# Kernel tuning notes

Hardware: AMD Instinct MI355X
Metric: run time of the kernel (lower is better)

## Reference

```python
import jax, jax.numpy as jnp
import numpy as np

D = 128
EPS = 1e-6


def setup_inputs() -> dict:
    key = jax.random.key(0)
    k1, k2, k3, k4 = jax.random.split(key, 4)
    N, NQ, NK = 32, 2048, 2048
    queries = jax.random.normal(k1, (N, NQ, D), dtype=jnp.float32)
    keys = jax.random.normal(k2, (N, NK, D), dtype=jnp.float32)
    values = jax.random.normal(k3, (N, NK, D), dtype=jnp.float32)
    # multiplicative (soft) mask in [0,1)
    mask = jax.random.uniform(k4, (N, NQ, NK), dtype=jnp.float32)
    return {"queries": queries, "keys": keys, "values": values, "mask": mask}


def reference(queries, keys, values, mask):
    # scaled dot-product scores: N x n_q x n_k
    scaled = jnp.einsum("bqd,bkd->bqk", queries, keys) / jnp.sqrt(jnp.float32(D))
    attn = jax.nn.softmax(scaled, axis=2)
    # post-softmax multiplicative masking + renormalization
    attn = attn * mask
    attn = attn / (jnp.sum(attn, axis=2, keepdims=True) + EPS)
    return jnp.einsum("bqk,bkd->bqd", attn, values)
```

## Files before the change

kernel.cpp:

```cpp
#include <hip/hip_runtime.h>

#define NB   32
#define NQL  2048
#define NKL  2048
#define DH   128
#define QBLK 128
#define KBLK 64
#define NT   (NKL / KBLK)
#define EPS  1e-6f

typedef __bf16 bf16x8 __attribute__((ext_vector_type(8)));
typedef __bf16 bf16x4 __attribute__((ext_vector_type(4)));
typedef float  f32x4  __attribute__((ext_vector_type(4)));

__global__ __launch_bounds__(256) void
prep_kv(const float* __restrict__ Kg, const float* __restrict__ Vg,
        unsigned short* __restrict__ Kimg, unsigned short* __restrict__ Vimg)
{
    __shared__ float T[64 * 132];
    const int t = threadIdx.x;
    if (blockIdx.x < NB * NT) {
        const int blk = blockIdx.x;
        const int rK  = t >> 2;
        const int x0  = (t & 3) * 32;
        const int swz = (rK & 7) << 3;
        const float* src = Kg + ((size_t)blk * 64 + rK) * DH;
        unsigned short* dst = Kimg + ((size_t)blk << 13) + rK * 128;
        #pragma unroll
        for (int i = 0; i < 4; ++i) {
            const int c0 = (x0 + i * 8) ^ swz;
            float4 a = *(const float4*)(src + c0);
            float4 c = *(const float4*)(src + c0 + 4);
            *(bf16x8*)(dst + x0 + i * 8) =
                (bf16x8){ (__bf16)a.x, (__bf16)a.y, (__bf16)a.z, (__bf16)a.w,
                          (__bf16)c.x, (__bf16)c.y, (__bf16)c.z, (__bf16)c.w };
        }
    } else {
        const int blk = blockIdx.x - NB * NT;
        {
            const int r  = t >> 2;
            const int c0 = (t & 3) * 32;
            const float* src = Vg + ((size_t)blk * 64 + r) * DH + c0;
            #pragma unroll
            for (int j = 0; j < 8; ++j)
                *(float4*)&T[r * 132 + c0 + j * 4] = *(const float4*)(src + j * 4);
        }
        __syncthreads();
        {
            const int dV  = t >> 1;
            const int yh  = (t & 1) * 32;
            const int swz = (dV & 7) << 3;
            unsigned short* dst = Vimg + ((size_t)blk << 13) + dV * 64 + yh;
            #pragma unroll
            for (int i = 0; i < 4; ++i) {
                const int ks = (yh + i * 8) ^ swz;
                bf16x8 o;
                #pragma unroll
                for (int j = 0; j < 8; ++j) o[j] = (__bf16)T[(ks + j) * 132 + dV];
                *(bf16x8*)(dst + i * 8) = o;
            }
        }
    }
}


#define GLL16(GSRC, LDST) \
    __builtin_amdgcn_global_load_lds( \
        (const __attribute__((address_space(1))) void*)(GSRC), \
        (__attribute__((address_space(3))) void*)(LDST), 16, 0, 0)

#define ISSUE_KV(KT, KB_, VB_) do { \
    const size_t tb_ = ((size_t)(b * 32 + (KT))) << 14; \
    const char* ksrc_ = KimgB + tb_ + woff + lby; \
    const char* vsrc_ = VimgB + tb_ + woff + lby; \
    char* kd_ = (char*)(KB_) + woff; \
    char* vd_ = (char*)(VB_) + woff; \
    GLL16(ksrc_ +    0, kd_ +    0);  GLL16(ksrc_ + 1024, kd_ + 1024); \
    GLL16(vsrc_ +    0, vd_ +    0);  GLL16(vsrc_ + 1024, vd_ + 1024); \
} while (0)

#define LOAD_M(K0, R0, R1, R2, R3) do { \
    const float* mb_ = mbase + (K0); \
    R0 = *(const float4*)(mb_ +  0);  R1 = *(const float4*)(mb_ + 16); \
    R2 = *(const float4*)(mb_ + 32);  R3 = *(const float4*)(mb_ + 48); \
} while (0)

#define COMPUTE(KB, VB, M0, M1, M2, M3) do { \
    f32x4 sacc[4]; \
    _Pragma("unroll") for (int m = 0; m < 4; ++m) sacc[m] = (f32x4){0.f,0.f,0.f,0.f}; \
    __builtin_amdgcn_s_setprio(1); \
    _Pragma("unroll") for (int m = 0; m < 4; ++m) { \
        _Pragma("unroll") for (int c = 0; c < 4; ++c) { \
            bf16x8 af = *(bf16x8*)&KB[(m * 16 + lq) * 128 + ((c * 32 + lg * 8) ^ swzL)]; \
            sacc[m] = __builtin_amdgcn_mfma_f32_16x16x32_bf16(af, qf[c], sacc[m], 0, 0, 0); \
        } \
    } \
    __builtin_amdgcn_s_setprio(0); \
    float mk_[16] = { M0.x, M0.y, M0.z, M0.w,  M1.x, M1.y, M1.z, M1.w, \
                      M2.x, M2.y, M2.z, M2.w,  M3.x, M3.y, M3.z, M3.w }; \
    float sv[4][4], tmax = -1e30f; \
    _Pragma("unroll") for (int m = 0; m < 4; ++m) \
        _Pragma("unroll") for (int r = 0; r < 4; ++r) { \
            sv[m][r] = sacc[m][r] * scale; \
            tmax = fmaxf(tmax, sv[m][r]); \
        } \
    tmax = fmaxf(tmax, __shfl_xor(tmax, 16)); \
    tmax = fmaxf(tmax, __shfl_xor(tmax, 32)); \
    if (!__all(tmax - m_run <= 8.f)) { \
        const float mnew_  = fmaxf(m_run, tmax); \
        const float alpha_ = __expf(m_run - mnew_); \
        m_run = mnew_;  z_part *= alpha_;  s_part *= alpha_; \
        float alr[4]; \
        _Pragma("unroll") for (int r = 0; r < 4; ++r) alr[r] = __shfl(alpha_, lg * 4 + r); \
        _Pragma("unroll") for (int n = 0; n < 8; ++n) \
            _Pragma("unroll") for (int r = 0; r < 4; ++r) oacc[n][r] *= alr[r]; \
    } \
    float zl = 0.f, sl = 0.f, pm[4][4]; \
    _Pragma("unroll") for (int m = 0; m < 4; ++m) \
        _Pragma("unroll") for (int r = 0; r < 4; ++r) { \
            float p = __expf(sv[m][r] - m_run); \
            zl += p; \
            float pq = p * mk_[m * 4 + r]; \
            sl += pq;  pm[m][r] = pq; \
        } \
    z_part += zl;  s_part += sl; \
    _Pragma("unroll") for (int kc = 0; kc < 2; ++kc) { \
        *(bf16x4*)&Ps[w][lq][lg * 4] = \
            (bf16x4){ (__bf16)pm[2*kc][0], (__bf16)pm[2*kc][1], \
                      (__bf16)pm[2*kc][2], (__bf16)pm[2*kc][3] }; \
        *(bf16x4*)&Ps[w][lq][16 + lg * 4] = \
            (bf16x4){ (__bf16)pm[2*kc+1][0], (__bf16)pm[2*kc+1][1], \
                      (__bf16)pm[2*kc+1][2], (__bf16)pm[2*kc+1][3] }; \
        bf16x8 pa = *(bf16x8*)&Ps[w][lq][lg * 8]; \
        __builtin_amdgcn_s_setprio(1); \
        _Pragma("unroll") for (int n = 0; n < 8; ++n) { \
            bf16x8 vv = *(bf16x8*)&VB[(n * 16 + lq) * 64 + ((kc * 32 + lg * 8) ^ swzL)]; \
            oacc[n] = __builtin_amdgcn_mfma_f32_16x16x32_bf16(pa, vv, oacc[n], 0, 0, 0); \
        } \
        __builtin_amdgcn_s_setprio(0); \
    } \
} while (0)

#define ITER(KT, KBc, VBc, KBn, VBn, MU0,MU1,MU2,MU3, ML0,ML1,ML2,ML3, LAST) do { \
    if (!(LAST)) { \
        ISSUE_KV((KT) + 1, KBn, VBn); \
        LOAD_M(((KT) + 1) * KBLK, ML0, ML1, ML2, ML3); \
    } \
    __builtin_amdgcn_sched_barrier(0); \
    COMPUTE(KBc, VBc, MU0, MU1, MU2, MU3); \
    if (!(LAST)) __syncthreads(); \
} while (0)

__global__ __launch_bounds__(512, 4) void
attn_main(const float* __restrict__ Qg, const unsigned short* __restrict__ Kimg,
          const unsigned short* __restrict__ Vimg, const float* __restrict__ Mg,
          float* __restrict__ Og)
{
    const int wg = ((blockIdx.x & 7) << 6) | (blockIdx.x >> 3);
    const int b  = wg >> 4;
    const int qt = wg & 15;

    const int t  = threadIdx.x;
    const int w  = t >> 6;
    const int l  = t & 63;
    const int lq = l & 15;
    const int lg = l >> 4;
    const int swzL = (lq & 7) << 3;
    const int woff = w * 2048;
    const int lby  = l * 16;

    __shared__ __align__(16) unsigned short Kb0[64 * 128];
    __shared__ __align__(16) unsigned short Kb1[64 * 128];
    __shared__ __align__(16) unsigned short Vb0[128 * 64];
    __shared__ __align__(16) unsigned short Vb1[128 * 64];
    __shared__ __align__(16) unsigned short Ps[8][16][40];

    const char* KimgB = (const char*)Kimg;
    const char* VimgB = (const char*)Vimg;

    const int qrow = qt * QBLK + w * 16 + lq;

    bf16x8 qf[4];
    {
        const float* qb = Qg + ((size_t)b * NQL + qrow) * DH;
        #pragma unroll
        for (int c = 0; c < 4; ++c) {
            const float* p = qb + c * 32 + lg * 8;
            float4 x = *(const float4*)(p);
            float4 y = *(const float4*)(p + 4);
            qf[c] = (bf16x8){ (__bf16)x.x, (__bf16)x.y, (__bf16)x.z, (__bf16)x.w,
                              (__bf16)y.x, (__bf16)y.y, (__bf16)y.z, (__bf16)y.w };
        }
    }

    float m_run = -1e30f, z_part = 0.f, s_part = 0.f;
    f32x4 oacc[8];
    #pragma unroll
    for (int n = 0; n < 8; ++n) oacc[n] = (f32x4){0.f, 0.f, 0.f, 0.f};

    const float* mbase = Mg + ((size_t)b * NQL + qrow) * NKL + lg * 4;
    const float scale = 0.08838834764831845f;

    float4 mA0, mA1, mA2, mA3, mB0, mB1, mB2, mB3;

    ISSUE_KV(0, Kb0, Vb0);
    LOAD_M(0, mA0, mA1, mA2, mA3);
    __syncthreads();

    for (int kt = 0; kt < NT - 2; kt += 2) {
        ITER(kt,     Kb0, Vb0, Kb1, Vb1, mA0,mA1,mA2,mA3, mB0,mB1,mB2,mB3, 0);
        ITER(kt + 1, Kb1, Vb1, Kb0, Vb0, mB0,mB1,mB2,mB3, mA0,mA1,mA2,mA3, 0);
    }
    ITER(NT - 2, Kb0, Vb0, Kb1, Vb1, mA0,mA1,mA2,mA3, mB0,mB1,mB2,mB3, 0);
    ITER(NT - 1, Kb1, Vb1, Kb0, Vb0, mB0,mB1,mB2,mB3, mA0,mA1,mA2,mA3, 1);

    float z = z_part + __shfl_xor(z_part, 16);
    z += __shfl_xor(z, 32);
    float s = s_part + __shfl_xor(s_part, 16);
    s += __shfl_xor(s, 32);
    const float inv = 1.f / (s + EPS * z);
    float ivr[4];
    #pragma unroll
    for (int r = 0; r < 4; ++r) ivr[r] = __shfl(inv, lg * 4 + r);

    float* ob = Og + ((size_t)b * NQL + qt * QBLK + w * 16) * DH;
    #pragma unroll
    for (int n = 0; n < 8; ++n)
        #pragma unroll
        for (int r = 0; r < 4; ++r)
            ob[(size_t)(lg * 4 + r) * DH + n * 16 + lq] = oacc[n][r] * ivr[r];
}

__global__ __launch_bounds__(256, 3) void
attn_fb(const float* __restrict__ Qg, const float* __restrict__ Kg,
        const float* __restrict__ Vg, const float* __restrict__ Mg,
        float* __restrict__ Og)
{
    const int wg = ((blockIdx.x & 7) << 7) | (blockIdx.x >> 3);
    const int b  = wg >> 5;
    const int q0 = (wg & 31) * 64;
    const int t  = threadIdx.x;
    const int w  = t >> 6;
    const int l  = t & 63;
    const int lq = l & 15;
    const int lg = l >> 4;
    __shared__ __align__(16) unsigned short Ks[64 * 128];
    __shared__ __align__(16) unsigned short Vs[128 * 64];
    __shared__ __align__(16) unsigned short Ps[4][16][72];
    const int rK   = t >> 2;
    const int cK   = (t & 3) * 32;
    const int dV   = t >> 1;
    const int khV  = t & 1;
    const int swzK = (rK & 7) << 3;
    const int swzV = (dV & 7) << 3;
    const int swzL = (lq & 7) << 3;
    const int qrow = q0 + w * 16 + lq;
    bf16x8 qf[4];
    {
        const float* qb = Qg + ((size_t)b * NQL + qrow) * DH;
        #pragma unroll
        for (int c = 0; c < 4; ++c) {
            const float* p = qb + c * 32 + lg * 8;
            float4 x = *(const float4*)(p);
            float4 y = *(const float4*)(p + 4);
            qf[c] = (bf16x8){ (__bf16)x.x, (__bf16)x.y, (__bf16)x.z, (__bf16)x.w,
                              (__bf16)y.x, (__bf16)y.y, (__bf16)y.z, (__bf16)y.w };
        }
    }
    float m_run = -1e30f, z_part = 0.f, s_part = 0.f;
    f32x4 oacc[8];
    #pragma unroll
    for (int n = 0; n < 8; ++n) oacc[n] = (f32x4){0.f, 0.f, 0.f, 0.f};
    const float* kbase = Kg + (size_t)b * NKL * DH;
    const float* vbase = Vg + (size_t)b * NKL * DH;
    const float* mbase = Mg + ((size_t)b * NQL + qrow) * NKL;
    const float scale = 0.08838834764831845f;
    for (int kt = 0; kt < NT; ++kt) {
        const int k0 = kt * KBLK;
        float mkf[16];
        {
            const float* mb = mbase + k0 + lg * 4;
            #pragma unroll
            for (int m = 0; m < 4; ++m) {
                float4 x = *(const float4*)(mb + m * 16);
                mkf[m*4+0]=x.x; mkf[m*4+1]=x.y; mkf[m*4+2]=x.z; mkf[m*4+3]=x.w;
            }
        }
        __syncthreads();
        {
            const float* kb = kbase + (size_t)(k0 + rK) * DH + cK;
            #pragma unroll
            for (int i = 0; i < 4; ++i) {
                float4 a = *(const float4*)(kb + i * 8);
                float4 c = *(const float4*)(kb + i * 8 + 4);
                *(bf16x8*)&Ks[rK * 128 + ((cK + i * 8) ^ swzK)] =
                    (bf16x8){ (__bf16)a.x, (__bf16)a.y, (__bf16)a.z, (__bf16)a.w,
                              (__bf16)c.x, (__bf16)c.y, (__bf16)c.z, (__bf16)c.w };
            }
            const float* vb = vbase + (size_t)(k0 + khV * 32) * DH + dV;
            #pragma unroll
            for (int i = 0; i < 4; ++i) {
                bf16x8 o;
                #pragma unroll
                for (int j = 0; j < 8; ++j) o[j] = (__bf16)vb[(i * 8 + j) * DH];
                *(bf16x8*)&Vs[dV * 64 + (((khV << 5) + i * 8) ^ swzV)] = o;
            }
        }
        __syncthreads();
        f32x4 sacc[4];
        #pragma unroll
        for (int m = 0; m < 4; ++m) sacc[m] = (f32x4){0.f,0.f,0.f,0.f};
        #pragma unroll
        for (int m = 0; m < 4; ++m)
            #pragma unroll
            for (int c = 0; c < 4; ++c) {
                bf16x8 af = *(bf16x8*)&Ks[(m * 16 + lq) * 128 + ((c * 32 + lg * 8) ^ swzL)];
                sacc[m] = __builtin_amdgcn_mfma_f32_16x16x32_bf16(af, qf[c], sacc[m], 0, 0, 0);
            }
        float sv[4][4], tmax = -1e30f;
        #pragma unroll
        for (int m = 0; m < 4; ++m)
            #pragma unroll
            for (int r = 0; r < 4; ++r) {
                sv[m][r] = sacc[m][r] * scale;
                tmax = fmaxf(tmax, sv[m][r]);
            }
        tmax = fmaxf(tmax, __shfl_xor(tmax, 16));
        tmax = fmaxf(tmax, __shfl_xor(tmax, 32));
        if (!__all(tmax - m_run <= 8.f)) {
            const float mnew  = fmaxf(m_run, tmax);
            const float alpha = __expf(m_run - mnew);
            m_run = mnew; z_part *= alpha; s_part *= alpha;
            float alr[4];
            #pragma unroll
            for (int r = 0; r < 4; ++r) alr[r] = __shfl(alpha, lg * 4 + r);
            #pragma unroll
            for (int n = 0; n < 8; ++n)
                #pragma unroll
                for (int r = 0; r < 4; ++r) oacc[n][r] *= alr[r];
        }
        float zl = 0.f, sl = 0.f, pm[4][4];
        #pragma unroll
        for (int m = 0; m < 4; ++m)
            #pragma unroll
            for (int r = 0; r < 4; ++r) {
                float p = __expf(sv[m][r] - m_run);
                zl += p;
                float pq = p * mkf[m * 4 + r];
                sl += pq; pm[m][r] = pq;
            }
        z_part += zl; s_part += sl;
        #pragma unroll
        for (int m = 0; m < 4; ++m)
            *(bf16x4*)&Ps[w][lq][m * 16 + lg * 4] =
                (bf16x4){ (__bf16)pm[m][0], (__bf16)pm[m][1], (__bf16)pm[m][2], (__bf16)pm[m][3] };
        #pragma unroll
        for (int kc = 0; kc < 2; ++kc) {
            bf16x8 pa = *(bf16x8*)&Ps[w][lq][kc * 32 + lg * 8];
            #pragma unroll
            for (int n = 0; n < 8; ++n) {
                bf16x8 vv = *(bf16x8*)&Vs[(n * 16 + lq) * 64 + ((kc * 32 + lg * 8) ^ swzL)];
                oacc[n] = __builtin_amdgcn_mfma_f32_16x16x32_bf16(pa, vv, oacc[n], 0, 0, 0);
            }
        }
    }
    float z = z_part + __shfl_xor(z_part, 16);
    z += __shfl_xor(z, 32);
    float s = s_part + __shfl_xor(s_part, 16);
    s += __shfl_xor(s, 32);
    const float inv = 1.f / (s + EPS * z);
    float ivr[4];
    #pragma unroll
    for (int r = 0; r < 4; ++r) ivr[r] = __shfl(inv, lg * 4 + r);
    float* ob = Og + ((size_t)b * NQL + q0 + w * 16) * DH;
    #pragma unroll
    for (int n = 0; n < 8; ++n)
        #pragma unroll
        for (int r = 0; r < 4; ++r)
            ob[(size_t)(lg * 4 + r) * DH + n * 16 + lq] = oacc[n][r] * ivr[r];
}

extern "C" void kernel_launch(void* const* d_in, const int* in_sizes, int n_in,
                              void* d_out, int out_size, void* d_ws, size_t ws_size,
                              hipStream_t stream)
{
    (void)in_sizes; (void)n_in; (void)out_size;
    const float* Q = (const float*)d_in[0];
    const float* K = (const float*)d_in[1];
    const float* V = (const float*)d_in[2];
    const float* M = (const float*)d_in[3];
    float* O = (float*)d_out;

    const size_t imgElems = (size_t)NB * NKL * DH;
    const size_t need     = 2 * imgElems * sizeof(unsigned short);

    if (ws_size >= need) {
        unsigned short* Kimg = (unsigned short*)d_ws;
        unsigned short* Vimg = Kimg + imgElems;
        prep_kv<<<dim3(2 * NB * NT), 256, 0, stream>>>(K, V, Kimg, Vimg);
        attn_main<<<dim3(NB * (NQL / QBLK)), 512, 0, stream>>>(Q, Kimg, Vimg, M, O);
    } else {
        attn_fb<<<dim3(NB * (NQL / 64)), 256, 0, stream>>>(Q, K, V, M, O);
    }
}
```

Before: 241.0 us.

## Use 64-row query tiles with single-buffered K/V and synchronous refill

Halves the query tile to 64 rows, runs 4 waves per block instead of 8, and doubles the grid. K/V tiles are now single-buffered in LDS, refilled between two barriers after each compute step, and each wave issues twice as many global-to-LDS loads. The mask prefetch stays double-buffered in registers. This cuts LDS use per block so more blocks fit per CU, but K/V load latency is no longer hidden behind compute, each K/V tile is fetched twice as often overall, and there are two barriers per tile.

After: 343.1 us. 42.4% more time.

```diff
diff --git a/kernel.cpp b/kernel.cpp
--- a/kernel.cpp
+++ b/kernel.cpp
@@ -4,7 +4,7 @@
 #define NQL  2048
 #define NKL  2048
 #define DH   128
-#define QBLK 128
+#define QBLK 64
 #define KBLK 64
 #define NT   (NKL / KBLK)
 #define EPS  1e-6f
@@ -69,14 +69,16 @@
         (const __attribute__((address_space(1))) void*)(GSRC), \
         (__attribute__((address_space(3))) void*)(LDST), 16, 0, 0)
 
-#define ISSUE_KV(KT, KB_, VB_) do { \
+#define ISSUE_KV(KT) do { \
     const size_t tb_ = ((size_t)(b * 32 + (KT))) << 14; \
     const char* ksrc_ = KimgB + tb_ + woff + lby; \
     const char* vsrc_ = VimgB + tb_ + woff + lby; \
-    char* kd_ = (char*)(KB_) + woff; \
-    char* vd_ = (char*)(VB_) + woff; \
+    char* kd_ = (char*)Kb + woff; \
+    char* vd_ = (char*)Vb + woff; \
     GLL16(ksrc_ +    0, kd_ +    0);  GLL16(ksrc_ + 1024, kd_ + 1024); \
+    GLL16(ksrc_ + 2048, kd_ + 2048);  GLL16(ksrc_ + 3072, kd_ + 3072); \
     GLL16(vsrc_ +    0, vd_ +    0);  GLL16(vsrc_ + 1024, vd_ + 1024); \
+    GLL16(vsrc_ + 2048, vd_ + 2048);  GLL16(vsrc_ + 3072, vd_ + 3072); \
 } while (0)
 
 #define LOAD_M(K0, R0, R1, R2, R3) do { \
@@ -85,13 +87,13 @@
     R2 = *(const float4*)(mb_ + 32);  R3 = *(const float4*)(mb_ + 48); \
 } while (0)
 
-#define COMPUTE(KB, VB, M0, M1, M2, M3) do { \
+#define COMPUTE(M0, M1, M2, M3) do { \
     f32x4 sacc[4]; \
     _Pragma("unroll") for (int m = 0; m < 4; ++m) sacc[m] = (f32x4){0.f,0.f,0.f,0.f}; \
     __builtin_amdgcn_s_setprio(1); \
     _Pragma("unroll") for (int m = 0; m < 4; ++m) { \
         _Pragma("unroll") for (int c = 0; c < 4; ++c) { \
-            bf16x8 af = *(bf16x8*)&KB[(m * 16 + lq) * 128 + ((c * 32 + lg * 8) ^ swzL)]; \
+            bf16x8 af = *(bf16x8*)&Kb[(m * 16 + lq) * 128 + ((c * 32 + lg * 8) ^ swzL)]; \
             sacc[m] = __builtin_amdgcn_mfma_f32_16x16x32_bf16(af, qf[c], sacc[m], 0, 0, 0); \
         } \
     } \
@@ -134,31 +136,21 @@
         bf16x8 pa = *(bf16x8*)&Ps[w][lq][lg * 8]; \
         __builtin_amdgcn_s_setprio(1); \
         _Pragma("unroll") for (int n = 0; n < 8; ++n) { \
-            bf16x8 vv = *(bf16x8*)&VB[(n * 16 + lq) * 64 + ((kc * 32 + lg * 8) ^ swzL)]; \
+            bf16x8 vv = *(bf16x8*)&Vb[(n * 16 + lq) * 64 + ((kc * 32 + lg * 8) ^ swzL)]; \
             oacc[n] = __builtin_amdgcn_mfma_f32_16x16x32_bf16(pa, vv, oacc[n], 0, 0, 0); \
         } \
         __builtin_amdgcn_s_setprio(0); \
     } \
 } while (0)
 
-#define ITER(KT, KBc, VBc, KBn, VBn, MU0,MU1,MU2,MU3, ML0,ML1,ML2,ML3, LAST) do { \
-    if (!(LAST)) { \
-        ISSUE_KV((KT) + 1, KBn, VBn); \
-        LOAD_M(((KT) + 1) * KBLK, ML0, ML1, ML2, ML3); \
-    } \
-    __builtin_amdgcn_sched_barrier(0); \
-    COMPUTE(KBc, VBc, MU0, MU1, MU2, MU3); \
-    if (!(LAST)) __syncthreads(); \
-} while (0)
-
-__global__ __launch_bounds__(512, 4) void
+__global__ __launch_bounds__(256, 4) void
 attn_main(const float* __restrict__ Qg, const unsigned short* __restrict__ Kimg,
           const unsigned short* __restrict__ Vimg, const float* __restrict__ Mg,
           float* __restrict__ Og)
 {
-    const int wg = ((blockIdx.x & 7) << 6) | (blockIdx.x >> 3);
-    const int b  = wg >> 4;
-    const int qt = wg & 15;
+    const int wg = ((blockIdx.x & 7) << 7) | (blockIdx.x >> 3);
+    const int b  = wg >> 5;
+    const int q0 = (wg & 31) * QBLK;
 
     const int t  = threadIdx.x;
     const int w  = t >> 6;
@@ -166,19 +158,17 @@
     const int lq = l & 15;
     const int lg = l >> 4;
     const int swzL = (lq & 7) << 3;
-    const int woff = w * 2048;
+    const int woff = w * 4096;
     const int lby  = l * 16;
 
-    __shared__ __align__(16) unsigned short Kb0[64 * 128];
-    __shared__ __align__(16) unsigned short Kb1[64 * 128];
-    __shared__ __align__(16) unsigned short Vb0[128 * 64];
-    __shared__ __align__(16) unsigned short Vb1[128 * 64];
-    __shared__ __align__(16) unsigned short Ps[8][16][40];
+    __shared__ __align__(16) unsigned short Kb[64 * 128];
+    __shared__ __align__(16) unsigned short Vb[128 * 64];
+    __shared__ __align__(16) unsigned short Ps[4][16][40];
 
     const char* KimgB = (const char*)Kimg;
     const char* VimgB = (const char*)Vimg;
 
-    const int qrow = qt * QBLK + w * 16 + lq;
+    const int qrow = q0 + w * 16 + lq;
 
     bf16x8 qf[4];
     {
@@ -203,16 +193,28 @@
 
     float4 mA0, mA1, mA2, mA3, mB0, mB1, mB2, mB3;
 
-    ISSUE_KV(0, Kb0, Vb0);
     LOAD_M(0, mA0, mA1, mA2, mA3);
+    ISSUE_KV(0);
     __syncthreads();
 
-    for (int kt = 0; kt < NT - 2; kt += 2) {
-        ITER(kt,     Kb0, Vb0, Kb1, Vb1, mA0,mA1,mA2,mA3, mB0,mB1,mB2,mB3, 0);
-        ITER(kt + 1, Kb1, Vb1, Kb0, Vb0, mB0,mB1,mB2,mB3, mA0,mA1,mA2,mA3, 0);
-    }
-    ITER(NT - 2, Kb0, Vb0, Kb1, Vb1, mA0,mA1,mA2,mA3, mB0,mB1,mB2,mB3, 0);
-    ITER(NT - 1, Kb1, Vb1, Kb0, Vb0, mB0,mB1,mB2,mB3, mA0,mA1,mA2,mA3, 1);
+    for (int kt = 0; kt < NT; kt += 2) {
+        if (kt + 1 < NT) LOAD_M((kt + 1) * KBLK, mB0, mB1, mB2, mB3);
+        COMPUTE(mA0, mA1, mA2, mA3);
+        if (kt + 1 < NT) {
+            __syncthreads();
+            ISSUE_KV(kt + 1);
+            __syncthreads();
+        }
+        if (kt + 1 < NT) {
+            if (kt + 2 < NT) LOAD_M((kt + 2) * KBLK, mA0, mA1, mA2, mA3);
+            COMPUTE(mB0, mB1, mB2, mB3);
+            if (kt + 2 < NT) {
+                __syncthreads();
+                ISSUE_KV(kt + 2);
+                __syncthreads();
+            }
+        }
+    }
 
     float z = z_part + __shfl_xor(z_part, 16);
     z += __shfl_xor(z, 32);
@@ -223,7 +225,7 @@
     #pragma unroll
     for (int r = 0; r < 4; ++r) ivr[r] = __shfl(inv, lg * 4 + r);
 
-    float* ob = Og + ((size_t)b * NQL + qt * QBLK + w * 16) * DH;
+    float* ob = Og + ((size_t)b * NQL + q0 + w * 16) * DH;
     #pragma unroll
     for (int n = 0; n < 8; ++n)
         #pragma unroll
@@ -398,7 +400,7 @@
         unsigned short* Kimg = (unsigned short*)d_ws;
         unsigned short* Vimg = Kimg + imgElems;
         prep_kv<<<dim3(2 * NB * NT), 256, 0, stream>>>(K, V, Kimg, Vimg);
-        attn_main<<<dim3(NB * (NQL / QBLK)), 512, 0, stream>>>(Q, Kimg, Vimg, M, O);
+        attn_main<<<dim3(NB * (NQL / QBLK)), 256, 0, stream>>>(Q, Kimg, Vimg, M, O);
     } else {
         attn_fb<<<dim3(NB * (NQL / 64)), 256, 0, stream>>>(Q, K, V, M, O);
     }
```
